# Performance work log

Hardware: AMD Instinct MI355X
Metric: run time of the kernel (lower is better)

The kernel has to match this reference:

```python
import jax, jax.numpy as jnp
import numpy as np

N = 50000      # nodes
E = 600000     # edges
D = 128        # hidden_dim (bottleneck=1)
G = 64         # graphs in batch
GN_EPS = 1e-5  # GraphNorm eps


def setup_inputs() -> dict:
    key = jax.random.key(0)
    ks = jax.random.split(key, 10)
    node_h = jax.random.normal(ks[0], (N, D), dtype=jnp.float32)
    edge_attr = jax.random.normal(ks[1], (E, D), dtype=jnp.float32)
    batch = jnp.sort(jax.random.randint(ks[2], (N,), 0, G)).astype(jnp.int64)
    edge_index = jax.random.randint(ks[3], (2, E), 0, N).astype(jnp.int64)
    # params: lin1, conv.lin (edge linear), conv.eps, GraphNorm(weight,bias,mean_scale)
    w1 = jax.random.normal(ks[4], (D, D), dtype=jnp.float32) * 0.02
    b1 = jnp.zeros((D,), dtype=jnp.float32)
    we = jax.random.normal(ks[5], (D, D), dtype=jnp.float32) * 0.02
    be = jnp.zeros((D,), dtype=jnp.float32)
    eps = jnp.zeros((), dtype=jnp.float32)  # train_eps, init 0
    gn_weight = jnp.ones((D,), dtype=jnp.float32)
    gn_bias = jnp.zeros((D,), dtype=jnp.float32)
    gn_mean_scale = jnp.ones((D,), dtype=jnp.float32)
    return {"node_h": node_h, "edge_attr": edge_attr, "batch": batch,
            "edge_index": edge_index, "w1": w1, "b1": b1, "we": we, "be": be,
            "eps": eps, "gn_weight": gn_weight, "gn_bias": gn_bias,
            "gn_mean_scale": gn_mean_scale}


def graph_norm(x, batch, weight, bias, mean_scale):
    ones = jnp.ones((x.shape[0],), dtype=x.dtype)
    cnt = jnp.maximum(jax.ops.segment_sum(ones, batch, num_segments=G), 1.0)[:, None]
    mean = jax.ops.segment_sum(x, batch, num_segments=G) / cnt
    out = x - mean[batch] * mean_scale
    var = jax.ops.segment_sum(out * out, batch, num_segments=G) / cnt
    std = jnp.sqrt(var + GN_EPS)
    return weight * out / std[batch] + bias


def reference(node_h, edge_attr, batch, edge_index, w1, b1, we, be, eps,
              gn_weight, gn_bias, gn_mean_scale):
    h = node_h @ w1.T + b1                                  # lin1: [N, D]
    src, dst = edge_index[0], edge_index[1]
    # GINEConvMod message: SiLU(x_j + lin(edge_attr)); gather -> add -> act
    msg = jax.nn.silu(h[src] + (edge_attr @ we.T + be))     # [E, D]
    agg = jax.ops.segment_sum(msg, dst, num_segments=N)     # scatter-add
    conv = (1.0 + eps) * h + agg                            # nn = Identity
    # dropout(p=0) and lin2=Identity are no-ops
    out = jax.nn.silu(conv)
    return graph_norm(out + node_h, batch, gn_weight, gn_bias, gn_mean_scale)
```

## Files before the change

kernel.cpp:

```cpp
#include <hip/hip_runtime.h>
#include <hip/hip_bf16.h>

#define NN 50000
#define NE 600000
#define DIM 128
#define NG 64
#define NCHUNK 98
#define NTILE_E 37500
#define EDGE_BLOCKS 1024

using bf16x8 = __attribute__((ext_vector_type(8))) __bf16;
using bf16x4 = __attribute__((ext_vector_type(4))) __bf16;
using f32x4  = __attribute__((ext_vector_type(4))) float;

__device__ __forceinline__ bf16x8 cvt8(const float* __restrict__ p) {
    f32x4 a = *(const f32x4*)p;
    f32x4 b = *(const f32x4*)(p + 4);
    bf16x8 r;
    #pragma unroll
    for (int i = 0; i < 4; ++i) { r[i] = (__bf16)a[i]; r[i + 4] = (__bf16)b[i]; }
    return r;
}

template<int NT>
__device__ __forceinline__ void stage_weights_swz(const float* __restrict__ W, __bf16* sW) {
    for (int i = threadIdx.x; i < 128 * 16; i += NT) {
        int row = i >> 4, seg = i & 15;
        *(bf16x8*)(&sW[row * 128 + ((seg ^ (row & 15)) << 3)]) = cvt8(W + row * 128 + seg * 8);
    }
    __syncthreads();
}

__device__ __forceinline__ bf16x8 ldsA(const __bf16* sW, int t, int col, int quad, int k0) {
    int chunk = ((k0 >> 3) + quad) ^ col;
    return *(const bf16x8*)(&sW[(t * 16 + col) * 128 + (chunk << 3)]);
}

__global__ __launch_bounds__(512) void gemm_bias(
    const float* __restrict__ X, const float* __restrict__ W,
    const float* __restrict__ bias, float* __restrict__ Y,
    __hip_bfloat16* __restrict__ Yb, int M)
{
    __shared__ __bf16 sW[128 * 128];
    stage_weights_swz<512>(W, sW);

    int wave = threadIdx.x >> 6, lane = threadIdx.x & 63;
    int col = lane & 15, quad = lane >> 4;
    int tile = (blockIdx.x * 8 + wave) * 16;
    if (tile >= M) return;

    f32x4 acc[8] = {};
    const float* xp = X + (size_t)(tile + col) * DIM + quad * 8;
    #pragma unroll
    for (int k0 = 0; k0 < 128; k0 += 32) {
        bf16x8 b = cvt8(xp + k0);
        #pragma unroll
        for (int t = 0; t < 8; ++t) {
            bf16x8 a = ldsA(sW, t, col, quad, k0);
            acc[t] = __builtin_amdgcn_mfma_f32_16x16x32_bf16(a, b, acc[t], 0, 0, 0);
        }
    }
    float* yp = Y + (size_t)(tile + col) * DIM + quad * 4;
    #pragma unroll
    for (int t = 0; t < 8; ++t) {
        f32x4 bv = *(const f32x4*)(bias + t * 16 + quad * 4);
        f32x4 o;
        #pragma unroll
        for (int r = 0; r < 4; ++r) o[r] = acc[t][r] + bv[r];
        *(f32x4*)(yp + t * 16) = o;
        #pragma unroll
        for (int r = 0; r < 4; ++r) acc[t][r] = o[r];
    }
    if (Yb) {
        __hip_bfloat16* ybp = Yb + (size_t)(tile + col) * DIM + quad * 32;
        #pragma unroll
        for (int tp = 0; tp < 4; ++tp) {
            bf16x8 o8;
            #pragma unroll
            for (int r = 0; r < 4; ++r) {
                o8[r]     = (__bf16)acc[2 * tp][r];
                o8[4 + r] = (__bf16)acc[2 * tp + 1][r];
            }
            *(bf16x8*)(ybp + tp * 8) = o8;
        }
    }
}

__global__ __launch_bounds__(256) void k_hist(const int* __restrict__ dst, int* __restrict__ deg) {
    int e = blockIdx.x * 256 + threadIdx.x;
    if (e < NE) atomicAdd(&deg[dst[e]], 1);
}

__global__ __launch_bounds__(256) void k_scan_a(const int* __restrict__ deg, int* __restrict__ chunkSum) {
    __shared__ int s[256];
    int c = blockIdx.x, t = threadIdx.x;
    int b = c * 512 + t;
    int v = (b < NN) ? deg[b] : 0;
    if (b + 256 < NN) v += deg[b + 256];
    s[t] = v; __syncthreads();
    for (int off = 128; off > 0; off >>= 1) {
        if (t < off) s[t] += s[t + off];
        __syncthreads();
    }
    if (t == 0) chunkSum[c] = s[0];
}

__global__ __launch_bounds__(128) void k_scan_b(const int* __restrict__ chunkSum,
                                                int* __restrict__ chunkOff, int* __restrict__ rowptr) {
    __shared__ int s[128];
    int t = threadIdx.x;
    int v = (t < NCHUNK) ? chunkSum[t] : 0;
    s[t] = v; __syncthreads();
    for (int off = 1; off < 128; off <<= 1) {
        int x = (t >= off) ? s[t - off] : 0;
        __syncthreads();
        s[t] += x;
        __syncthreads();
    }
    chunkOff[t] = s[t] - v;
    if (t == 0) rowptr[NN] = NE;
}

__global__ __launch_bounds__(512) void k_scan_c(const int* __restrict__ deg,
                                                const int* __restrict__ chunkOff,
                                                int* __restrict__ rowptr, int* __restrict__ pos) {
    __shared__ int s[512];
    int c = blockIdx.x, t = threadIdx.x;
    int i = c * 512 + t;
    int v = (i < NN) ? deg[i] : 0;
    s[t] = v; __syncthreads();
    for (int off = 1; off < 512; off <<= 1) {
        int x = (t >= off) ? s[t - off] : 0;
        __syncthreads();
        s[t] += x;
        __syncthreads();
    }
    if (i < NN) { rowptr[i] = chunkOff[c] + s[t] - v; pos[i] = 0; }
}

__global__ __launch_bounds__(256) void k_slot(const int* __restrict__ dst,
                                              const int* __restrict__ rowptr,
                                              int* __restrict__ pos, int* __restrict__ slot) {
    int e = blockIdx.x * 256 + threadIdx.x;
    if (e >= NE) return;
    int d = dst[e];
    int p = atomicAdd(&pos[d], 1);
    slot[e] = rowptr[d] + p;
}

__global__ __launch_bounds__(512) void edge_msg_sorted(
    const float* __restrict__ EA, const float* __restrict__ W,
    const float* __restrict__ bias,
    const int* __restrict__ src, const int* __restrict__ slot,
    const __hip_bfloat16* __restrict__ Hb, __hip_bfloat16* __restrict__ MSG)
{
    __shared__ __bf16 sW[128 * 128];
    stage_weights_swz<512>(W, sW);

    int wave = threadIdx.x >> 6, lane = threadIdx.x & 63;
    int col = lane & 15, quad = lane >> 4;
    int wstride = gridDim.x * 8;

    for (int ti = blockIdx.x * 8 + wave; ti < NTILE_E; ti += wstride) {
        int e  = ti * 16 + col;
        int s  = src[e];
        int sl = slot[e];

        f32x4 acc[8] = {};
        const float* xp = EA + (size_t)e * DIM + quad * 8;
        #pragma unroll
        for (int k0 = 0; k0 < 128; k0 += 32) {
            bf16x8 b = cvt8(xp + k0);
            #pragma unroll
            for (int t = 0; t < 8; ++t) {
                bf16x8 a = ldsA(sW, t, col, quad, k0);
                acc[t] = __builtin_amdgcn_mfma_f32_16x16x32_bf16(a, b, acc[t], 0, 0, 0);
            }
        }

        const __hip_bfloat16* hp = Hb + (size_t)s * DIM + quad * 32;
        bf16x8 hv4[4];
        #pragma unroll
        for (int tp = 0; tp < 4; ++tp) hv4[tp] = *(const bf16x8*)(hp + tp * 8);

        __hip_bfloat16* mp = MSG + (size_t)sl * DIM + quad * 4;
        #pragma unroll
        for (int t = 0; t < 8; ++t) {
            f32x4 bv = *(const f32x4*)(bias + t * 16 + quad * 4);
            bf16x4 o;
            #pragma unroll
            for (int r = 0; r < 4; ++r) {
                float hf = __bfloat162float((__hip_bfloat16)hv4[t >> 1][(t & 1) * 4 + r]);
                float v = acc[t][r] + bv[r] + hf;
                v = v / (1.f + __expf(-v));
                o[r] = (__bf16)v;
            }
            *(bf16x4*)(mp + t * 16) = o;
        }
    }
}

__global__ __launch_bounds__(128) void k_gather_stats(
    const __hip_bfloat16* __restrict__ MSG, const int* __restrict__ rowptr,
    float* __restrict__ H, const float* __restrict__ node_h,
    const float* __restrict__ epsp, const int* __restrict__ batch,
    float* __restrict__ SUMS, float* __restrict__ SQS,
    float* __restrict__ CNT, int npb)
{
    int d = threadIdx.x;
    int n0 = blockIdx.x * npb;
    int nend = min(n0 + npb, NN);
    if (n0 >= NN) return;
    float epsv = 1.f + epsp[0];
    int cur_g = batch[n0];
    float run = 0.f, run2 = 0.f; int runlen = 0;
    for (int n = n0; n < nend; ++n) {
        int g = batch[n];
        if (g != cur_g) {
            atomicAdd(&SUMS[cur_g * DIM + d], run);
            atomicAdd(&SQS[cur_g * DIM + d], run2);
            if (d == 0) atomicAdd(&CNT[cur_g], (float)runlen);
            run = 0.f; run2 = 0.f; runlen = 0; cur_g = g;
        }
        int s = rowptr[n], epos = rowptr[n + 1];
        const __hip_bfloat16* mp = MSG + (size_t)s * DIM + d;
        float a0 = 0.f, a1 = 0.f, a2 = 0.f, a3 = 0.f;
        int e = s;
        for (; e + 4 <= epos; e += 4, mp += 4 * DIM) {
            a0 += __bfloat162float(mp[0]);
            a1 += __bfloat162float(mp[DIM]);
            a2 += __bfloat162float(mp[2 * DIM]);
            a3 += __bfloat162float(mp[3 * DIM]);
        }
        for (; e < epos; ++e, mp += DIM) a0 += __bfloat162float(mp[0]);
        float agg = (a0 + a1) + (a2 + a3);
        size_t idx = (size_t)n * DIM + d;
        float v = epsv * H[idx] + agg;
        v = v / (1.f + __expf(-v));
        v += node_h[idx];
        H[idx] = v;
        run += v; run2 += v * v; runlen++;
    }
    atomicAdd(&SUMS[cur_g * DIM + d], run);
    atomicAdd(&SQS[cur_g * DIM + d], run2);
    if (d == 0) atomicAdd(&CNT[cur_g], (float)runlen);
}

__global__ __launch_bounds__(128) void finalize(
    const float* __restrict__ X, const int* __restrict__ batch,
    const float* __restrict__ msc,
    const float* __restrict__ SUMS, const float* __restrict__ SQS,
    const float* __restrict__ CNT,
    const float* __restrict__ gw, const float* __restrict__ gb,
    float* __restrict__ OUT, int npb)
{
    int d = threadIdx.x;
    int n0 = blockIdx.x * npb;
    int nend = min(n0 + npb, NN);
    if (n0 >= NN) return;
    float ms = msc[d], wd = gw[d], bd = gb[d];
    int cur_g = -1;
    float mean = 0.f, rstd = 0.f;
    for (int n = n0; n < nend; ++n) {
        int g = batch[n];
        if (g != cur_g) {
            cur_g = g;
            float c = fmaxf(CNT[g], 1.f);
            mean = SUMS[g * DIM + d] / c;
            float ex2 = SQS[g * DIM + d] / c;
            float var = ex2 - mean * mean * ms * (2.f - ms);
            rstd = rsqrtf(fmaxf(var, 0.f) + 1e-5f);
        }
        size_t idx = (size_t)n * DIM + d;
        float v = X[idx] - mean * ms;
        OUT[idx] = wd * v * rstd + bd;
    }
}

__global__ __launch_bounds__(128) void stats_pass(
    const float* __restrict__ X, const int* __restrict__ batch,
    float* __restrict__ SUMS, float* __restrict__ SQS,
    float* __restrict__ CNT, int npb)
{
    int d = threadIdx.x;
    int n0 = blockIdx.x * npb;
    int nend = min(n0 + npb, NN);
    if (n0 >= NN) return;
    int cur_g = batch[n0];
    float run = 0.f, run2 = 0.f; int runlen = 0;
    for (int n = n0; n < nend; ++n) {
        int g = batch[n];
        if (g != cur_g) {
            atomicAdd(&SUMS[cur_g * DIM + d], run);
            atomicAdd(&SQS[cur_g * DIM + d], run2);
            if (d == 0) atomicAdd(&CNT[cur_g], (float)runlen);
            run = 0.f; run2 = 0.f; runlen = 0; cur_g = g;
        }
        float x = X[(size_t)n * DIM + d];
        run += x; run2 += x * x; runlen++;
    }
    atomicAdd(&SUMS[cur_g * DIM + d], run);
    atomicAdd(&SQS[cur_g * DIM + d], run2);
    if (d == 0) atomicAdd(&CNT[cur_g], (float)runlen);
}

__global__ __launch_bounds__(512) void edge_msg_atomic(
    const float* __restrict__ EA, const float* __restrict__ W,
    const float* __restrict__ bias,
    const int* __restrict__ src, const int* __restrict__ dst,
    const float* __restrict__ H, float* __restrict__ AGG)
{
    __shared__ __bf16 sW[128 * 128];
    int wave = threadIdx.x >> 6, lane = threadIdx.x & 63;
    int col = lane & 15, quad = lane >> 4;
    int tile = (blockIdx.x * 8 + wave) * 16;
    bool active = (tile < NE);
    int e = active ? (tile + col) : 0;
    int s = src[e], dd = dst[e];

    stage_weights_swz<512>(W, sW);
    if (!active) return;

    f32x4 acc[8] = {};
    const float* xp = EA + (size_t)e * DIM + quad * 8;
    #pragma unroll
    for (int k0 = 0; k0 < 128; k0 += 32) {
        bf16x8 b = cvt8(xp + k0);
        #pragma unroll
        for (int t = 0; t < 8; ++t) {
            bf16x8 a = ldsA(sW, t, col, quad, k0);
            acc[t] = __builtin_amdgcn_mfma_f32_16x16x32_bf16(a, b, acc[t], 0, 0, 0);
        }
    }
    const float* hp = H + (size_t)s * DIM + quad * 4;
    f32x4 hv[8];
    #pragma unroll
    for (int t = 0; t < 8; ++t) hv[t] = *(const f32x4*)(hp + t * 16);

    float* ap = AGG + (size_t)dd * DIM + quad * 4;
    #pragma unroll
    for (int t = 0; t < 8; ++t) {
        f32x4 bv = *(const f32x4*)(bias + t * 16 + quad * 4);
        #pragma unroll
        for (int r = 0; r < 4; ++r) {
            float v = acc[t][r] + bv[r] + hv[t][r];
            v = v / (1.f + __expf(-v));
            atomicAdd(&ap[t * 16 + r], v);
        }
    }
}

__global__ __launch_bounds__(128) void fuse_x_atomic(
    float* __restrict__ H, const float* __restrict__ AGG,
    const float* __restrict__ node_h, const float* __restrict__ epsp, int npb)
{
    int d = threadIdx.x;
    int n0 = blockIdx.x * npb;
    int nend = min(n0 + npb, NN);
    if (n0 >= NN) return;
    float epsv = 1.f + epsp[0];
    for (int n = n0; n < nend; ++n) {
        size_t idx = (size_t)n * DIM + d;
        float v = epsv * H[idx] + AGG[idx];
        v = v / (1.f + __expf(-v));
        H[idx] = v + node_h[idx];
    }
}

extern "C" void kernel_launch(void* const* d_in, const int* in_sizes, int n_in,
                              void* d_out, int out_size, void* d_ws, size_t ws_size,
                              hipStream_t stream) {
    const float* node_h    = (const float*)d_in[0];
    const float* edge_attr = (const float*)d_in[1];
    const int*   batch     = (const int*)d_in[2];
    const int*   eidx      = (const int*)d_in[3];
    const float* w1        = (const float*)d_in[4];
    const float* b1        = (const float*)d_in[5];
    const float* we        = (const float*)d_in[6];
    const float* be        = (const float*)d_in[7];
    const float* eps       = (const float*)d_in[8];
    const float* gnw       = (const float*)d_in[9];
    const float* gnb       = (const float*)d_in[10];
    const float* gnms      = (const float*)d_in[11];
    const int* src = eidx, * dst = eidx + NE;

    char* base = (char*)d_ws;
    float* H = (float*)base;

    size_t oMSG   = 25600000;
    size_t oROW   = oMSG + 153600000;
    size_t oDEG   = oROW + 200064;
    size_t oSUMS  = oDEG + 200000;
    size_t oSQS   = oSUMS + 32768;
    size_t oCNT   = oSQS + 32768;
    size_t oSLOT  = oCNT + 256;
    size_t oCSA   = oSLOT + 2400000;
    size_t oCSB   = oCSA + 512;
    size_t oHB    = oCSB + 512;
    size_t needed = oHB + 12800000;

    bool fast = ws_size >= needed;

    if (fast) {
        __hip_bfloat16* MSG = (__hip_bfloat16*)(base + oMSG);
        int* rowptr = (int*)(base + oROW);
        int* deg    = (int*)(base + oDEG);
        float* SUMS = (float*)(base + oSUMS);
        float* SQS  = (float*)(base + oSQS);
        float* CNT  = (float*)(base + oCNT);
        int* slot   = (int*)(base + oSLOT);
        int* csum   = (int*)(base + oCSA);
        int* coff   = (int*)(base + oCSB);
        __hip_bfloat16* Hb = (__hip_bfloat16*)(base + oHB);

        hipMemsetAsync(deg, 0, 200000 + 32768 + 32768 + 256, stream);

        gemm_bias<<<391, 512, 0, stream>>>(node_h, w1, b1, H, Hb, NN);
        k_hist  <<<(NE + 255) / 256, 256, 0, stream>>>(dst, deg);
        k_scan_a<<<NCHUNK, 256, 0, stream>>>(deg, csum);
        k_scan_b<<<1, 128, 0, stream>>>(csum, coff, rowptr);
        k_scan_c<<<NCHUNK, 512, 0, stream>>>(deg, coff, rowptr, deg );
        k_slot  <<<(NE + 255) / 256, 256, 0, stream>>>(dst, rowptr, deg, slot);
        edge_msg_sorted<<<EDGE_BLOCKS, 512, 0, stream>>>(edge_attr, we, be, src, slot, Hb, MSG);
        k_gather_stats<<<3125, 128, 0, stream>>>(MSG, rowptr, H, node_h, eps, batch,
                                                 SUMS, SQS, CNT, 16);
        finalize<<<3125, 128, 0, stream>>>(H, batch, gnms, SUMS, SQS, CNT, gnw, gnb,
                                           (float*)d_out, 16);
    } else {
        float* AGG  = H + 6400000;
        float* SUMS = H + 12800000;
        float* SQS  = SUMS + NG * DIM;
        float* CNT  = SQS + NG * DIM;
        hipMemsetAsync(AGG, 0, (size_t)(6400000 + NG * DIM * 2 + NG) * sizeof(float), stream);
        gemm_bias<<<391, 512, 0, stream>>>(node_h, w1, b1, H, nullptr, NN);
        edge_msg_atomic<<<4688, 512, 0, stream>>>(edge_attr, we, be, src, dst, H, AGG);
        fuse_x_atomic<<<3125, 128, 0, stream>>>(H, AGG, node_h, eps, 16);
        stats_pass<<<3125, 128, 0, stream>>>(H, batch, SUMS, SQS, CNT, 16);
        finalize  <<<3125, 128, 0, stream>>>(H, batch, gnms, SUMS, SQS, CNT, gnw, gnb,
                                             (float*)d_out, 16);
    }
}
```

Before: 660.4 us.

## Software-pipeline edge message tiles, use nontemporal memory ops, refine gather granularity

The edge message kernel now prefetches the next tile's edge attributes, gathered hidden rows and indices into registers while the current tile runs its MFMA and SiLU epilogue, with the first loads issued before weight staging. The edge grid drops to 512 blocks. Edge attribute loads, message stores and gather-side message loads use nontemporal hints, and the gather adds an 8-way unrolled accumulation with a cheaper bf16-to-float conversion. Gather and finalize run with 8 nodes per block and twice the blocks. The prefetch raises register pressure, which may lower occupancy, and the halved grid may leave fewer waves to hide latency.

Result: slower. 761.3 us (+15.3%).

```diff
diff --git a/kernel.cpp b/kernel.cpp
--- a/kernel.cpp
+++ b/kernel.cpp
@@ -7,7 +7,7 @@
 #define NG 64
 #define NCHUNK 98
 #define NTILE_E 37500
-#define EDGE_BLOCKS 1024
+#define EDGE_BLOCKS 512
 
 using bf16x8 = __attribute__((ext_vector_type(8))) __bf16;
 using bf16x4 = __attribute__((ext_vector_type(4))) __bf16;
@@ -20,6 +20,17 @@
     #pragma unroll
     for (int i = 0; i < 4; ++i) { r[i] = (__bf16)a[i]; r[i + 4] = (__bf16)b[i]; }
     return r;
+}
+
+__device__ __forceinline__ bf16x8 cvt8v(f32x4 a, f32x4 b) {
+    bf16x8 r;
+    #pragma unroll
+    for (int i = 0; i < 4; ++i) { r[i] = (__bf16)a[i]; r[i + 4] = (__bf16)b[i]; }
+    return r;
+}
+
+__device__ __forceinline__ float bu2f(unsigned short u) {
+    return __uint_as_float(((unsigned int)u) << 16);
 }
 
 template<int NT>
@@ -148,6 +159,57 @@
     slot[e] = rowptr[d] + p;
 }
 
+struct ETile {
+    f32x4  ea[8];
+    bf16x8 hv[4];
+};
+
+__device__ __forceinline__ void load_tile_data(
+    const float* __restrict__ EA, const __hip_bfloat16* __restrict__ Hb,
+    int e, int s, int quad, ETile& T)
+{
+    const float* xp = EA + (size_t)e * DIM + quad * 8;
+    #pragma unroll
+    for (int k = 0; k < 4; ++k) {
+        T.ea[2 * k]     = __builtin_nontemporal_load((const f32x4*)(xp + 32 * k));
+        T.ea[2 * k + 1] = __builtin_nontemporal_load((const f32x4*)(xp + 32 * k + 4));
+    }
+    const __hip_bfloat16* hp = Hb + (size_t)s * DIM + quad * 32;
+    #pragma unroll
+    for (int tp = 0; tp < 4; ++tp) T.hv[tp] = *(const bf16x8*)(hp + tp * 8);
+}
+
+__device__ __forceinline__ void compute_store_tile(
+    const __bf16* sW, const float* __restrict__ bias,
+    __hip_bfloat16* __restrict__ MSG, const ETile& T, int sl,
+    int col, int quad)
+{
+    f32x4 acc[8] = {};
+    #pragma unroll
+    for (int kk = 0; kk < 4; ++kk) {
+        bf16x8 b = cvt8v(T.ea[2 * kk], T.ea[2 * kk + 1]);
+        #pragma unroll
+        for (int t = 0; t < 8; ++t) {
+            bf16x8 a = ldsA(sW, t, col, quad, kk * 32);
+            acc[t] = __builtin_amdgcn_mfma_f32_16x16x32_bf16(a, b, acc[t], 0, 0, 0);
+        }
+    }
+    __hip_bfloat16* mp = MSG + (size_t)sl * DIM + quad * 4;
+    #pragma unroll
+    for (int t = 0; t < 8; ++t) {
+        f32x4 bv = *(const f32x4*)(bias + t * 16 + quad * 4);
+        bf16x4 o;
+        #pragma unroll
+        for (int r = 0; r < 4; ++r) {
+            float hf = (float)T.hv[t >> 1][(t & 1) * 4 + r];
+            float v = acc[t][r] + bv[r] + hf;
+            v = v / (1.f + __expf(-v));
+            o[r] = (__bf16)v;
+        }
+        __builtin_nontemporal_store(o, (bf16x4*)(mp + t * 16));
+    }
+}
+
 __global__ __launch_bounds__(512) void edge_msg_sorted(
     const float* __restrict__ EA, const float* __restrict__ W,
     const float* __restrict__ bias,
@@ -155,48 +217,38 @@
     const __hip_bfloat16* __restrict__ Hb, __hip_bfloat16* __restrict__ MSG)
 {
     __shared__ __bf16 sW[128 * 128];
-    stage_weights_swz<512>(W, sW);
 
     int wave = threadIdx.x >> 6, lane = threadIdx.x & 63;
     int col = lane & 15, quad = lane >> 4;
     int wstride = gridDim.x * 8;
 
-    for (int ti = blockIdx.x * 8 + wave; ti < NTILE_E; ti += wstride) {
-        int e  = ti * 16 + col;
-        int s  = src[e];
-        int sl = slot[e];
-
-        f32x4 acc[8] = {};
-        const float* xp = EA + (size_t)e * DIM + quad * 8;
-        #pragma unroll
-        for (int k0 = 0; k0 < 128; k0 += 32) {
-            bf16x8 b = cvt8(xp + k0);
-            #pragma unroll
-            for (int t = 0; t < 8; ++t) {
-                bf16x8 a = ldsA(sW, t, col, quad, k0);
-                acc[t] = __builtin_amdgcn_mfma_f32_16x16x32_bf16(a, b, acc[t], 0, 0, 0);
-            }
-        }
-
-        const __hip_bfloat16* hp = Hb + (size_t)s * DIM + quad * 32;
-        bf16x8 hv4[4];
-        #pragma unroll
-        for (int tp = 0; tp < 4; ++tp) hv4[tp] = *(const bf16x8*)(hp + tp * 8);
-
-        __hip_bfloat16* mp = MSG + (size_t)sl * DIM + quad * 4;
-        #pragma unroll
-        for (int t = 0; t < 8; ++t) {
-            f32x4 bv = *(const f32x4*)(bias + t * 16 + quad * 4);
-            bf16x4 o;
-            #pragma unroll
-            for (int r = 0; r < 4; ++r) {
-                float hf = __bfloat162float((__hip_bfloat16)hv4[t >> 1][(t & 1) * 4 + r]);
-                float v = acc[t][r] + bv[r] + hf;
-                v = v / (1.f + __expf(-v));
-                o[r] = (__bf16)v;
-            }
-            *(bf16x4*)(mp + t * 16) = o;
-        }
+    int ti0 = blockIdx.x * 8 + wave;
+    int e0 = ti0 * 16 + col;
+    int s0 = src[e0], sl0 = slot[e0];
+    int ti1 = ti0 + wstride;
+    bool m1 = ti1 < NTILE_E;
+    int s1 = 0, sl1 = 0;
+    if (m1) { int e1 = ti1 * 16 + col; s1 = src[e1]; sl1 = slot[e1]; }
+
+    stage_weights_swz<512>(W, sW);
+
+    ETile T0;
+    load_tile_data(EA, Hb, e0, s0, quad, T0);
+
+    while (true) {
+        ETile T1;
+        if (m1) load_tile_data(EA, Hb, ti1 * 16 + col, s1, quad, T1);
+        int ti2 = ti1 + wstride;
+        bool m2 = ti2 < NTILE_E;
+        int s2 = 0, sl2 = 0;
+        if (m2) { int e2 = ti2 * 16 + col; s2 = src[e2]; sl2 = slot[e2]; }
+
+        compute_store_tile(sW, bias, MSG, T0, sl0, col, quad);
+
+        if (!m1) break;
+        T0 = T1; sl0 = sl1;
+        s1 = s2; sl1 = sl2;
+        ti1 = ti2; m1 = m2;
     }
 }
 
@@ -223,17 +275,29 @@
             run = 0.f; run2 = 0.f; runlen = 0; cur_g = g;
         }
         int s = rowptr[n], epos = rowptr[n + 1];
-        const __hip_bfloat16* mp = MSG + (size_t)s * DIM + d;
+        const unsigned short* mp = (const unsigned short*)MSG + (size_t)s * DIM + d;
         float a0 = 0.f, a1 = 0.f, a2 = 0.f, a3 = 0.f;
+        float a4 = 0.f, a5 = 0.f, a6 = 0.f, a7 = 0.f;
         int e = s;
+        for (; e + 8 <= epos; e += 8, mp += 8 * DIM) {
+            a0 += bu2f(__builtin_nontemporal_load(mp));
+            a1 += bu2f(__builtin_nontemporal_load(mp + DIM));
+            a2 += bu2f(__builtin_nontemporal_load(mp + 2 * DIM));
+            a3 += bu2f(__builtin_nontemporal_load(mp + 3 * DIM));
+            a4 += bu2f(__builtin_nontemporal_load(mp + 4 * DIM));
+            a5 += bu2f(__builtin_nontemporal_load(mp + 5 * DIM));
+            a6 += bu2f(__builtin_nontemporal_load(mp + 6 * DIM));
+            a7 += bu2f(__builtin_nontemporal_load(mp + 7 * DIM));
+        }
         for (; e + 4 <= epos; e += 4, mp += 4 * DIM) {
-            a0 += __bfloat162float(mp[0]);
-            a1 += __bfloat162float(mp[DIM]);
-            a2 += __bfloat162float(mp[2 * DIM]);
-            a3 += __bfloat162float(mp[3 * DIM]);
-        }
-        for (; e < epos; ++e, mp += DIM) a0 += __bfloat162float(mp[0]);
-        float agg = (a0 + a1) + (a2 + a3);
+            a0 += bu2f(__builtin_nontemporal_load(mp));
+            a1 += bu2f(__builtin_nontemporal_load(mp + DIM));
+            a2 += bu2f(__builtin_nontemporal_load(mp + 2 * DIM));
+            a3 += bu2f(__builtin_nontemporal_load(mp + 3 * DIM));
+        }
+        for (; e < epos; ++e, mp += DIM)
+            a0 += bu2f(__builtin_nontemporal_load(mp));
+        float agg = ((a0 + a1) + (a2 + a3)) + ((a4 + a5) + (a6 + a7));
         size_t idx = (size_t)n * DIM + d;
         float v = epsv * H[idx] + agg;
         v = v / (1.f + __expf(-v));
@@ -422,10 +486,10 @@
         k_scan_c<<<NCHUNK, 512, 0, stream>>>(deg, coff, rowptr, deg );
         k_slot  <<<(NE + 255) / 256, 256, 0, stream>>>(dst, rowptr, deg, slot);
         edge_msg_sorted<<<EDGE_BLOCKS, 512, 0, stream>>>(edge_attr, we, be, src, slot, Hb, MSG);
-        k_gather_stats<<<3125, 128, 0, stream>>>(MSG, rowptr, H, node_h, eps, batch,
-                                                 SUMS, SQS, CNT, 16);
-        finalize<<<3125, 128, 0, stream>>>(H, batch, gnms, SUMS, SQS, CNT, gnw, gnb,
-                                           (float*)d_out, 16);
+        k_gather_stats<<<6250, 128, 0, stream>>>(MSG, rowptr, H, node_h, eps, batch,
+                                                 SUMS, SQS, CNT, 8);
+        finalize<<<6250, 128, 0, stream>>>(H, batch, gnms, SUMS, SQS, CNT, gnw, gnb,
+                                           (float*)d_out, 8);
     } else {
         float* AGG  = H + 6400000;
         float* SUMS = H + 12800000;
```
